# Kernel optimization log

Measured on AMD Instinct MI355X. Metric: run time of the kernel, lower is better.

## Reference

```python
import math
import jax, jax.numpy as jnp
import numpy as np

N_FREQS = 16
MAX_PERIOD = 4096.0
INJECTION_SCALE = 1.0


def setup_inputs() -> dict:
    key = jax.random.key(0)
    ks = jax.random.split(key, 5)
    B, L, D, K = 4, 8192, 1024, 2
    read_in = K * 2 * N_FREQS  # 64
    x = jax.random.normal(ks[0], (B, L, D), dtype=jnp.float32)
    # Linear weights stored as (in, out) so y = x @ W + b (== torch x @ W.T + b)
    inc_w = jax.random.normal(ks[1], (D, K), dtype=jnp.float32) * 0.02
    inc_b = jnp.full((K,), -2.0, dtype=jnp.float32)   # nn.init.constant_(inc_proj.bias, -2.0)
    reset_w = jax.random.normal(ks[2], (D, K), dtype=jnp.float32) * 0.02
    reset_b = jnp.full((K,), -5.0, dtype=jnp.float32)  # nn.init.constant_(reset_proj.bias, -5.0)
    read_w = jax.random.normal(ks[3], (read_in, D), dtype=jnp.float32) * 0.02
    read_b = jnp.zeros((D,), dtype=jnp.float32)
    return {"x": x, "inc_w": inc_w, "inc_b": inc_b, "reset_w": reset_w,
            "reset_b": reset_b, "read_w": read_w, "read_b": read_b}


def reference(x, inc_w, inc_b, reset_w, reset_b, read_w, read_b):
    # Gates from hidden state
    inc_logits = x @ inc_w + inc_b        # (B, L, K)
    reset_logits = x @ reset_w + reset_b  # (B, L, K)
    inc = jax.nn.sigmoid(inc_logits)
    keep = 1.0 - jax.nn.sigmoid(reset_logits)

    # Diagonal linear recurrence c[t] = keep[t]*c[t-1] + inc[t]
    # expressed as an associative scan over affine maps f(x) = k*x + i.
    def combine(left, right):
        kl, il = left
        kr, ir = right
        return (kl * kr, ir + kr * il)

    _, counters = jax.lax.associative_scan(combine, (keep, inc), axis=1)  # (B, L, K)

    # Sinusoidal readout: (B, L, K) -> (B, L, K*2*n_freqs)
    freqs = jnp.exp(jnp.linspace(0.0, math.log(MAX_PERIOD), N_FREQS)).astype(x.dtype)
    sc = counters[..., None] / freqs                       # (B, L, K, F)
    emb = jnp.concatenate([jnp.sin(sc), jnp.cos(sc)], -1)  # (B, L, K, 2F)
    B, L, K, _ = emb.shape
    emb = emb.reshape(B, L, K * 2 * N_FREQS)

    injection = INJECTION_SCALE * (emb @ read_w + read_b)  # (B, L, d_model)
    return injection, inc_logits, counters
```

## Files before the change

kernel.cpp:

```cpp
#include <hip/hip_runtime.h>

#define B_    4
#define L_    8192
#define D_    1024
#define ROWS_ 32768
#define NCH_  128

typedef __attribute__((ext_vector_type(8))) short  short8;
typedef __attribute__((ext_vector_type(4))) float  floatx4;

__device__ __forceinline__ unsigned short f2bf(float f){
  unsigned int u = __float_as_uint(f);
  u += 0x7fffu + ((u >> 16) & 1u);
  return (unsigned short)(u >> 16);
}

__global__ __launch_bounds__(512) void k_gates(
    const float* __restrict__ x,
    const float* __restrict__ inc_w, const float* __restrict__ inc_b,
    const float* __restrict__ reset_w, const float* __restrict__ reset_b,
    float* __restrict__ out_incl,
    float* __restrict__ cl, float* __restrict__ kc,
    float* __restrict__ sumP, float* __restrict__ sumQ)
{
  __shared__ float s_keep[128];
  __shared__ float s_inc[128];
  const int blk  = blockIdx.x;
  const int b    = blk >> 7;
  const int ch   = blk & 127;
  const int tid  = threadIdx.x;
  const int w    = tid >> 6;
  const int lane = tid & 63;

  float4 wia[4], wib[4], wra[4], wrb[4];
  #pragma unroll
  for (int i = 0; i < 4; ++i){
    const int d0 = i*256 + lane*4;
    const float4* pi = (const float4*)(inc_w + d0*2);
    wia[i] = pi[0]; wib[i] = pi[1];
    const float4* pr = (const float4*)(reset_w + d0*2);
    wra[i] = pr[0]; wrb[i] = pr[1];
  }
  const float bi0 = inc_b[0], bi1 = inc_b[1];
  const float br0 = reset_b[0], br1 = reset_b[1];

  const int row0 = b*L_ + ch*64 + w*8;
  float4 xc[4], xn[4];
  {
    const float4* xr = (const float4*)(x + (size_t)row0 * D_);
    #pragma unroll
    for (int i = 0; i < 4; ++i) xc[i] = xr[i*64 + lane];
  }
  #pragma unroll
  for (int r = 0; r < 8; ++r){
    if (r < 7){
      const float4* xr = (const float4*)(x + (size_t)(row0 + r + 1) * D_);
      #pragma unroll
      for (int i = 0; i < 4; ++i) xn[i] = xr[i*64 + lane];
    }
    float ai0=0.f, ai1=0.f, ar0=0.f, ar1=0.f;
    #pragma unroll
    for (int i = 0; i < 4; ++i){
      const float4 v = xc[i];
      ai0 += v.x*wia[i].x + v.y*wia[i].z + v.z*wib[i].x + v.w*wib[i].z;
      ai1 += v.x*wia[i].y + v.y*wia[i].w + v.z*wib[i].y + v.w*wib[i].w;
      ar0 += v.x*wra[i].x + v.y*wra[i].z + v.z*wrb[i].x + v.w*wrb[i].z;
      ar1 += v.x*wra[i].y + v.y*wra[i].w + v.z*wrb[i].y + v.w*wrb[i].w;
    }
    #pragma unroll
    for (int m = 1; m < 64; m <<= 1){
      ai0 += __shfl_xor(ai0, m);
      ai1 += __shfl_xor(ai1, m);
      ar0 += __shfl_xor(ar0, m);
      ar1 += __shfl_xor(ar1, m);
    }
    if (lane == 0){
      const int row = row0 + r;
      const float il0 = ai0 + bi0, il1 = ai1 + bi1;
      const float rl0 = ar0 + br0, rl1 = ar1 + br1;
      out_incl[(size_t)row*2 + 0] = il0;
      out_incl[(size_t)row*2 + 1] = il1;
      const int lr = w*8 + r;
      s_inc [lr*2+0] = 1.f / (1.f + __expf(-il0));
      s_inc [lr*2+1] = 1.f / (1.f + __expf(-il1));
      s_keep[lr*2+0] = 1.f - 1.f / (1.f + __expf(-rl0));
      s_keep[lr*2+1] = 1.f - 1.f / (1.f + __expf(-rl1));
    }
    #pragma unroll
    for (int i = 0; i < 4; ++i) xc[i] = xn[i];
  }
  __syncthreads();

  if (tid < 128){
    const int k = w;
    float P = s_keep[lane*2 + k];
    float Q = s_inc [lane*2 + k];
    #pragma unroll
    for (int ofs = 1; ofs < 64; ofs <<= 1){
      const float Pp = __shfl_up(P, ofs);
      const float Qp = __shfl_up(Q, ofs);
      if (lane >= ofs){ Q = Q + P * Qp; P = P * Pp; }
    }
    const int row = b*L_ + ch*64 + lane;
    cl[(size_t)row*2 + k] = Q;
    kc[(size_t)row*2 + k] = P;
    if (lane == 63){
      const int seq = b*2 + k;
      sumP[seq*NCH_ + ch] = P;
      sumQ[seq*NCH_ + ch] = Q;
    }
  }
}

__global__ __launch_bounds__(512) void k_scan2(
    const float* __restrict__ sumP, const float* __restrict__ sumQ,
    float* __restrict__ carry,
    const float* __restrict__ read_w, unsigned short* __restrict__ Bt)
{
  if (blockIdx.x == 0){
    const int tid  = threadIdx.x;
    const int seq  = tid >> 6;
    const int lane = tid & 63;
    const float* P0 = sumP + seq*NCH_;
    const float* Q0 = sumQ + seq*NCH_;
    float P = P0[lane], Q = Q0[lane];
    #pragma unroll
    for (int ofs = 1; ofs < 64; ofs <<= 1){
      const float Pp = __shfl_up(P, ofs);
      const float Qp = __shfl_up(Q, ofs);
      if (lane >= ofs){ Q = Q + P * Qp; P = P * Pp; }
    }
    if (lane == 0) carry[seq*NCH_ + 0] = 0.f;
    carry[seq*NCH_ + lane + 1] = Q;
    const float Pc = __shfl(P, 63);
    const float Qc = __shfl(Q, 63);
    float P2 = P0[64 + lane], Q2 = Q0[64 + lane];
    #pragma unroll
    for (int ofs = 1; ofs < 64; ofs <<= 1){
      const float Pp = __shfl_up(P2, ofs);
      const float Qp = __shfl_up(Q2, ofs);
      if (lane >= ofs){ Q2 = Q2 + P2 * Qp; P2 = P2 * Pp; }
    }
    Q2 = Q2 + P2 * Qc;
    if (lane < 63) carry[seq*NCH_ + 65 + lane] = Q2;
  } else {
    const int idx = (blockIdx.x - 1)*512 + threadIdx.x;
    const int n  = idx >> 6;
    const int kk = idx & 63;
    Bt[idx] = f2bf(read_w[(size_t)kk*D_ + n]);
  }
}

__global__ __launch_bounds__(256) void k_fused(
    const float* __restrict__ cl, const float* __restrict__ kc,
    const float* __restrict__ carry,
    const unsigned short* __restrict__ Bt,
    const float* __restrict__ read_b,
    float* __restrict__ out_cnt, float* __restrict__ out)
{
  const int tid  = threadIdx.x;
  const int w    = tid >> 6;
  const int lane = tid & 63;
  const int rowBase = blockIdx.x * 16;
  const int m    = lane & 15;
  const int quad = lane >> 4;

  const int row = rowBase + m;
  const int b   = row >> 13;
  const int ch  = (row & (L_ - 1)) >> 6;
  const float2 clv = *(const float2*)(cl + (size_t)row*2);
  const float2 kcv = *(const float2*)(kc + (size_t)row*2);
  const float c0 = clv.x + kcv.x * carry[(b*2+0)*NCH_ + ch];
  const float c1 = clv.y + kcv.y * carry[(b*2+1)*NCH_ + ch];
  if (w == 0 && lane < 16){
    ((float2*)out_cnt)[row] = make_float2(c0, c1);
  }

  const float TWO_PI_INV = 0.15915494309189535f;
  const float STEP = 0.5743491774985175f;
  float invf = (quad & 1) ? 0.011841535573494211f  : 1.0f;
  const bool use_cos = (quad >> 1) != 0;
  short8 a0, a1;
  #pragma unroll
  for (int j = 0; j < 8; ++j){
    float r0 = c0 * invf * TWO_PI_INV; r0 -= floorf(r0);
    float r1 = c1 * invf * TWO_PI_INV; r1 -= floorf(r1);
    const float e0 = use_cos ? __builtin_amdgcn_cosf(r0) : __builtin_amdgcn_sinf(r0);
    const float e1 = use_cos ? __builtin_amdgcn_cosf(r1) : __builtin_amdgcn_sinf(r1);
    a0[j] = (short)f2bf(e0);
    a1[j] = (short)f2bf(e1);
    invf *= STEP;
  }

  const int colBase = w * 256;
  floatx4 acc[16];
  #pragma unroll
  for (int ct = 0; ct < 16; ++ct) acc[ct] = (floatx4){0.f,0.f,0.f,0.f};
  #pragma unroll
  for (int ct = 0; ct < 16; ++ct){
    const int n = colBase + ct*16 + m;
    const short8* bp = (const short8*)(Bt + (size_t)n * 64);
    const short8 b0 = bp[quad];
    const short8 b1 = bp[4 + quad];
    acc[ct] = __builtin_amdgcn_mfma_f32_16x16x32_bf16(a0, b0, acc[ct], 0, 0, 0);
    acc[ct] = __builtin_amdgcn_mfma_f32_16x16x32_bf16(a1, b1, acc[ct], 0, 0, 0);
  }

  #pragma unroll
  for (int ct = 0; ct < 16; ++ct){
    const int col  = colBase + ct*16 + m;
    const float bias = read_b[col];
    #pragma unroll
    for (int r = 0; r < 4; ++r){
      const int orow = rowBase + quad*4 + r;
      out[(size_t)orow*D_ + col] = acc[ct][r] + bias;
    }
  }
}

extern "C" void kernel_launch(void* const* d_in, const int* in_sizes, int n_in,
                              void* d_out, int out_size, void* d_ws, size_t ws_size,
                              hipStream_t stream) {
  const float* x       = (const float*)d_in[0];
  const float* inc_w   = (const float*)d_in[1];
  const float* inc_b   = (const float*)d_in[2];
  const float* reset_w = (const float*)d_in[3];
  const float* reset_b = (const float*)d_in[4];
  const float* read_w  = (const float*)d_in[5];
  const float* read_b  = (const float*)d_in[6];

  float* out      = (float*)d_out;
  float* out_incl = out + (size_t)ROWS_ * D_;
  float* out_cnt  = out_incl + ROWS_ * 2;

  char* ws = (char*)d_ws;
  float* cl    = (float*)(ws + 0);
  float* kc    = (float*)(ws + 262144);
  float* sumP  = (float*)(ws + 524288);
  float* sumQ  = (float*)(ws + 528384);
  float* carry = (float*)(ws + 532480);
  unsigned short* Bt  = (unsigned short*)(ws + 540672);

  k_gates<<<dim3(512),  dim3(512), 0, stream>>>(x, inc_w, inc_b, reset_w, reset_b,
                                                out_incl, cl, kc, sumP, sumQ);
  k_scan2<<<dim3(129),  dim3(512), 0, stream>>>(sumP, sumQ, carry, read_w, Bt);
  k_fused<<<dim3(2048), dim3(256), 0, stream>>>(cl, kc, carry, Bt, read_b,
                                                out_cnt, out);
}
```

Baseline: 264.5 us.

## Eliminate scan kernel: fold weight conversion into gates, recompute carries per block

Removes the middle k_scan2 launch. The bf16 transpose of read_w moves into 32 extra blocks of k_gates, each thread converting four values. Every k_fused block now redoes the chunk-level carry scan itself with two wavefronts and passes the result through shared memory. This trades one launch and a global round trip for redundant scan work and a __syncthreads in each of the 2048 fused blocks.

```diff
diff --git a/kernel.cpp b/kernel.cpp
--- a/kernel.cpp
+++ b/kernel.cpp
@@ -21,11 +21,25 @@
     const float* __restrict__ reset_w, const float* __restrict__ reset_b,
     float* __restrict__ out_incl,
     float* __restrict__ cl, float* __restrict__ kc,
-    float* __restrict__ sumP, float* __restrict__ sumQ)
+    float* __restrict__ sumP, float* __restrict__ sumQ,
+    const float* __restrict__ read_w, unsigned short* __restrict__ Bt)
 {
+  const int blk  = blockIdx.x;
+  if (blk >= 512){
+    const int idx0 = ((blk - 512)*512 + threadIdx.x)*4;
+    const int n  = idx0 >> 6;
+    const int kk = idx0 & 63;
+    ushort4 v;
+    v.x = f2bf(read_w[(size_t)(kk+0)*D_ + n]);
+    v.y = f2bf(read_w[(size_t)(kk+1)*D_ + n]);
+    v.z = f2bf(read_w[(size_t)(kk+2)*D_ + n]);
+    v.w = f2bf(read_w[(size_t)(kk+3)*D_ + n]);
+    *(ushort4*)(Bt + idx0) = v;
+    return;
+  }
+
   __shared__ float s_keep[128];
   __shared__ float s_inc[128];
-  const int blk  = blockIdx.x;
   const int b    = blk >> 7;
   const int ch   = blk & 127;
   const int tid  = threadIdx.x;
@@ -112,15 +126,25 @@
   }
 }
 
-__global__ __launch_bounds__(512) void k_scan2(
+__global__ __launch_bounds__(256) void k_fused(
+    const float* __restrict__ cl, const float* __restrict__ kc,
     const float* __restrict__ sumP, const float* __restrict__ sumQ,
-    float* __restrict__ carry,
-    const float* __restrict__ read_w, unsigned short* __restrict__ Bt)
+    const unsigned short* __restrict__ Bt,
+    const float* __restrict__ read_b,
+    float* __restrict__ out_cnt, float* __restrict__ out)
 {
-  if (blockIdx.x == 0){
-    const int tid  = threadIdx.x;
-    const int seq  = tid >> 6;
-    const int lane = tid & 63;
+  __shared__ float s_carry[2];
+  const int tid  = threadIdx.x;
+  const int w    = tid >> 6;
+  const int lane = tid & 63;
+  const int rowBase = blockIdx.x * 16;
+  const int b   = rowBase >> 13;
+  const int ch  = (rowBase & (L_ - 1)) >> 6;
+  const int m    = lane & 15;
+  const int quad = lane >> 4;
+
+  if (w < 2){
+    const int seq = b*2 + w;
     const float* P0 = sumP + seq*NCH_;
     const float* Q0 = sumQ + seq*NCH_;
     float P = P0[lane], Q = Q0[lane];
@@ -130,9 +154,8 @@
       const float Qp = __shfl_up(Q, ofs);
       if (lane >= ofs){ Q = Q + P * Qp; P = P * Pp; }
     }
-    if (lane == 0) carry[seq*NCH_ + 0] = 0.f;
-    carry[seq*NCH_ + lane + 1] = Q;
-    const float Pc = __shfl(P, 63);
+    float carry = 0.f;
+    if (ch > 0 && ch <= 64) carry = __shfl(Q, ch-1);
     const float Qc = __shfl(Q, 63);
     float P2 = P0[64 + lane], Q2 = Q0[64 + lane];
     #pragma unroll
@@ -142,36 +165,18 @@
       if (lane >= ofs){ Q2 = Q2 + P2 * Qp; P2 = P2 * Pp; }
     }
     Q2 = Q2 + P2 * Qc;
-    if (lane < 63) carry[seq*NCH_ + 65 + lane] = Q2;
-  } else {
-    const int idx = (blockIdx.x - 1)*512 + threadIdx.x;
-    const int n  = idx >> 6;
-    const int kk = idx & 63;
-    Bt[idx] = f2bf(read_w[(size_t)kk*D_ + n]);
-  }
-}
-
-__global__ __launch_bounds__(256) void k_fused(
-    const float* __restrict__ cl, const float* __restrict__ kc,
-    const float* __restrict__ carry,
-    const unsigned short* __restrict__ Bt,
-    const float* __restrict__ read_b,
-    float* __restrict__ out_cnt, float* __restrict__ out)
-{
-  const int tid  = threadIdx.x;
-  const int w    = tid >> 6;
-  const int lane = tid & 63;
-  const int rowBase = blockIdx.x * 16;
-  const int m    = lane & 15;
-  const int quad = lane >> 4;
+    if (ch >= 65) carry = __shfl(Q2, ch-65);
+    if (lane == 0) s_carry[w] = carry;
+  }
+  __syncthreads();
+  const float carry0 = s_carry[0];
+  const float carry1 = s_carry[1];
 
   const int row = rowBase + m;
-  const int b   = row >> 13;
-  const int ch  = (row & (L_ - 1)) >> 6;
   const float2 clv = *(const float2*)(cl + (size_t)row*2);
   const float2 kcv = *(const float2*)(kc + (size_t)row*2);
-  const float c0 = clv.x + kcv.x * carry[(b*2+0)*NCH_ + ch];
-  const float c1 = clv.y + kcv.y * carry[(b*2+1)*NCH_ + ch];
+  const float c0 = clv.x + kcv.x * carry0;
+  const float c1 = clv.y + kcv.y * carry1;
   if (w == 0 && lane < 16){
     ((float2*)out_cnt)[row] = make_float2(c0, c1);
   }
@@ -238,12 +243,11 @@
   float* kc    = (float*)(ws + 262144);
   float* sumP  = (float*)(ws + 524288);
   float* sumQ  = (float*)(ws + 528384);
-  float* carry = (float*)(ws + 532480);
-  unsigned short* Bt  = (unsigned short*)(ws + 540672);
-
-  k_gates<<<dim3(512),  dim3(512), 0, stream>>>(x, inc_w, inc_b, reset_w, reset_b,
-                                                out_incl, cl, kc, sumP, sumQ);
-  k_scan2<<<dim3(129),  dim3(512), 0, stream>>>(sumP, sumQ, carry, read_w, Bt);
-  k_fused<<<dim3(2048), dim3(256), 0, stream>>>(cl, kc, carry, Bt, read_b,
+  unsigned short* Bt  = (unsigned short*)(ws + 532480);
+
+  k_gates<<<dim3(544),  dim3(512), 0, stream>>>(x, inc_w, inc_b, reset_w, reset_b,
+                                                out_incl, cl, kc, sumP, sumQ,
+                                                read_w, Bt);
+  k_fused<<<dim3(2048), dim3(256), 0, stream>>>(cl, kc, sumP, sumQ, Bt, read_b,
                                                 out_cnt, out);
 }
```

Result: no change. 263.8 us (-0.3%).
